# Kernel tuning notes

Measured on AMD Instinct MI355X. Metric: run time of the kernel, lower is better.

The kernel has to match this reference:

```python
import jax, jax.numpy as jnp
import numpy as np

B, T = 48, 88200          # batch of 2 s clips at internal_sr=44100
N_EXC, N_LOOP = 6, 2      # exc_order+1, loop_order+1


def invert_lpc(y, A):
    """x[t] = y[t] + sum_{k=1..N} A[:, t, k-1] * y[t-k]  (zi = 0).
    y: (B,T), A: (B,T,N) -> (B,T). Vectorized time-varying FIR."""
    Bs, Ts = y.shape
    N = A.shape[2]
    yp = jnp.pad(y, ((0, 0), (N, 0)))  # N leading zeros = zero initial state
    # shifts[:, t, k-1] = y[t-k]
    shifts = jnp.stack([yp[:, N - k:N - k + Ts] for k in range(1, N + 1)], axis=2)
    return y + jnp.sum(A * shifts, axis=2)


def sample_wise_lpc(x, A):
    """Time-varying all-pole IIR: y[t] = x[t] - sum_{k=1..N} A[:, t, k-1]*y[t-k].
    Sequential recurrence over T via lax.scan. x: (B,T), A: (B,T,N)."""
    Bs, Ts = x.shape
    N = A.shape[2]

    def step(carry, inp):
        # carry: (B,N) = [y[t-1], ..., y[t-N]]
        xt, at = inp  # (B,), (B,N)
        yt = xt - jnp.sum(at * carry, axis=1)
        new_carry = jnp.concatenate([yt[:, None], carry[:, :-1]], axis=1)
        return new_carry, yt

    carry0 = jnp.zeros((Bs, N), x.dtype)
    _, ys = jax.lax.scan(step, carry0, (x.T, jnp.swapaxes(A, 0, 1)))
    return ys.T  # (B,T)


def setup_inputs() -> dict:
    key = jax.random.key(0)
    k1, k2, k3 = jax.random.split(key, 3)
    y = jax.random.normal(k1, (B, T), dtype=jnp.float32)
    # excitation (FIR-inverse) coefficients: mild, zero-centered
    A_exc = (jax.random.uniform(k2, (B, T, N_EXC), dtype=jnp.float32) - 0.5) * 0.2
    # loop (all-pole) coefficients kept small so the IIR recurrence is stable
    A_loop = (jax.random.uniform(k3, (B, T, N_LOOP), dtype=jnp.float32) - 0.5) * 0.5
    return {"y": y, "A_exc": A_exc, "A_loop": A_loop}


def reference(y, A_exc, A_loop):
    # Core DiffKS pipeline kernel: inverse LPC (feed-forward comb/loop inversion)
    # followed by the sample-wise recursive LPC resynthesis (Karplus-Strong loop).
    x = invert_lpc(y, A_exc)
    return sample_wise_lpc(x, A_loop)
```

## Files before the change

kernel.cpp:

```cpp
#include <hip/hip_runtime.h>


#define T_LEN 88200
#define B_N   48
#define OUT_W 224
#define WUP   32
#define NCH   394
#define WPB   4

__device__ __forceinline__ float4 zero4() { return make_float4(0.f, 0.f, 0.f, 0.f); }

__device__ __forceinline__ float4 ld_guard(const float* p, int t) {
    if (t >= 0 && t + 3 < T_LEN) return *(const float4*)(p + t);
    return zero4();
}

__global__ __launch_bounds__(256, 5) void diffks_kernel(
    const float* __restrict__ y, const float* __restrict__ A_exc,
    const float* __restrict__ A_loop, float* __restrict__ out) {
    const int tid  = threadIdx.x;
    const int widx = tid >> 6;
    const int lane = tid & 63;
    const int w = blockIdx.x * WPB + widx;
    const int b = w / NCH;
    const int c = w - b * NCH;
    const int s  = c * OUT_W;
    const int w0 = s - WUP;
    const int t0 = w0 + 4 * lane;

    const float* yb  = y      + (size_t)b * T_LEN;
    const float* aeb = A_exc  + (size_t)b * T_LEN * 6;
    const float* alb = A_loop + (size_t)b * T_LEN * 2;
    float*       ob  = out    + (size_t)b * T_LEN;

    const bool valid = (t0 >= 0) && (t0 + 3 < T_LEN);
    float4 yv, ae0, ae1, ae2, ae3, ae4, ae5, al0, al1;
    if (valid) {
        yv = *(const float4*)(yb + t0);
        const float4* pae = (const float4*)(aeb + (size_t)t0 * 6);
        ae0 = pae[0]; ae1 = pae[1]; ae2 = pae[2];
        ae3 = pae[3]; ae4 = pae[4]; ae5 = pae[5];
        const float4* pal = (const float4*)(alb + (size_t)t0 * 2);
        al0 = pal[0]; al1 = pal[1];
    } else {
        yv = ae0 = ae1 = ae2 = ae3 = ae4 = ae5 = al0 = al1 = zero4();
    }

    float4 ymid, ylo;
    ymid.x = __shfl_up(yv.x, 1, 64); ymid.y = __shfl_up(yv.y, 1, 64);
    ymid.z = __shfl_up(yv.z, 1, 64); ymid.w = __shfl_up(yv.w, 1, 64);
    ylo.x  = __shfl_up(yv.x, 2, 64); ylo.y  = __shfl_up(yv.y, 2, 64);
    ylo.z  = __shfl_up(yv.z, 2, 64); ylo.w  = __shfl_up(yv.w, 2, 64);
    if (lane == 0) ymid = ld_guard(yb, t0 - 4);
    if (lane <= 1) ylo  = ld_guard(yb, t0 - 8);

    float yw[12] = { ylo.x, ylo.y, ylo.z, ylo.w,
                     ymid.x, ymid.y, ymid.z, ymid.w,
                     yv.x, yv.y, yv.z, yv.w };
    float aef[24] = { ae0.x, ae0.y, ae0.z, ae0.w, ae1.x, ae1.y, ae1.z, ae1.w,
                      ae2.x, ae2.y, ae2.z, ae2.w, ae3.x, ae3.y, ae3.z, ae3.w,
                      ae4.x, ae4.y, ae4.z, ae4.w, ae5.x, ae5.y, ae5.z, ae5.w };
    float alf[8]  = { al0.x, al0.y, al0.z, al0.w, al1.x, al1.y, al1.z, al1.w };

    float xs[4], a1s[4], a2s[4];
    float p00 = 1.f, p01 = 0.f, p10 = 0.f, p11 = 1.f, c0 = 0.f, c1 = 0.f;
#pragma unroll
    for (int j = 0; j < 4; ++j) {
        float xv = yw[8 + j];
#pragma unroll
        for (int k = 1; k <= 6; ++k)
            xv = fmaf(aef[j * 6 + (k - 1)], yw[8 + j - k], xv);
        xs[j] = xv;
        const float a1 = alf[j * 2], a2 = alf[j * 2 + 1];
        a1s[j] = a1; a2s[j] = a2;
        const float n00 = fmaf(-a1, p00, -a2 * p10);
        const float n01 = fmaf(-a1, p01, -a2 * p11);
        p10 = p00; p11 = p01; p00 = n00; p01 = n01;
        const float nc0 = fmaf(-a1, c0, fmaf(-a2, c1, xv));
        c1 = c0; c0 = nc0;
    }

#pragma unroll
    for (int d = 1; d <= 4; d <<= 1) {
        const float q00 = __shfl_up(p00, d, 64), q01 = __shfl_up(p01, d, 64);
        const float q10 = __shfl_up(p10, d, 64), q11 = __shfl_up(p11, d, 64);
        const float qc0 = __shfl_up(c0, d, 64),  qc1 = __shfl_up(c1, d, 64);
        if (lane >= d) {
            const float m00 = fmaf(p00, q00, p01 * q10);
            const float m01 = fmaf(p00, q01, p01 * q11);
            const float m10 = fmaf(p10, q00, p11 * q10);
            const float m11 = fmaf(p10, q01, p11 * q11);
            const float nc0 = fmaf(p00, qc0, fmaf(p01, qc1, c0));
            const float nc1 = fmaf(p10, qc0, fmaf(p11, qc1, c1));
            p00 = m00; p01 = m01; p10 = m10; p11 = m11; c0 = nc0; c1 = nc1;
        }
    }
    {
        const float qc0 = __shfl_up(c0, 8, 64), qc1 = __shfl_up(c1, 8, 64);
        if (lane >= 8) {
            const float nc0 = fmaf(p00, qc0, fmaf(p01, qc1, c0));
            const float nc1 = fmaf(p10, qc0, fmaf(p11, qc1, c1));
            c0 = nc0; c1 = nc1;
        }
    }

    float y1 = __shfl_up(c0, 1, 64);
    float y2 = __shfl_up(c1, 1, 64);
    if (lane == 0) { y1 = 0.f; y2 = 0.f; }
    float ov[4];
#pragma unroll
    for (int j = 0; j < 4; ++j) {
        const float yt = fmaf(-a1s[j], y1, fmaf(-a2s[j], y2, xs[j]));
        y2 = y1; y1 = yt;
        ov[j] = yt;
    }

    if (lane >= 8 && t0 < T_LEN)
        *(float4*)(ob + t0) = make_float4(ov[0], ov[1], ov[2], ov[3]);
}

extern "C" void kernel_launch(void* const* d_in, const int* in_sizes, int n_in,
                              void* d_out, int out_size, void* d_ws, size_t ws_size,
                              hipStream_t stream) {
    const float* y      = (const float*)d_in[0];
    const float* A_exc  = (const float*)d_in[1];
    const float* A_loop = (const float*)d_in[2];
    float* out = (float*)d_out;

    const int waves = B_N * NCH;
    const int grid  = waves / WPB;
    diffks_kernel<<<grid, 256, 0, stream>>>(y, A_exc, A_loop, out);
}
```

Measured before the change: 190.1 us.

## Process eight samples per lane to widen chunks and cut warm-up overhead

Each lane now handles 8 consecutive samples instead of 4, so a wave covers 480 output samples per chunk rather than 224. The fixed 32-sample warm-up is amortized over more outputs, which cuts redundant loads and compute, and the scan needs fewer shuffle steps. Halo y values are now loaded directly from memory instead of shuffled from neighbouring lanes. Register pressure per lane rises, so the occupancy hint is lowered from 5 to 4 blocks per CU, and fewer waves are launched.

```diff
diff --git a/kernel.cpp b/kernel.cpp
--- a/kernel.cpp
+++ b/kernel.cpp
@@ -3,19 +3,19 @@
 
 #define T_LEN 88200
 #define B_N   48
-#define OUT_W 224
+#define OUT_W 480
 #define WUP   32
-#define NCH   394
+#define NCH   184
 #define WPB   4
 
 __device__ __forceinline__ float4 zero4() { return make_float4(0.f, 0.f, 0.f, 0.f); }
 
-__device__ __forceinline__ float4 ld_guard(const float* p, int t) {
+__device__ __forceinline__ float4 ld_g(const float* __restrict__ p, int t) {
     if (t >= 0 && t + 3 < T_LEN) return *(const float4*)(p + t);
     return zero4();
 }
 
-__global__ __launch_bounds__(256, 5) void diffks_kernel(
+__global__ __launch_bounds__(256, 4) void diffks_kernel(
     const float* __restrict__ y, const float* __restrict__ A_exc,
     const float* __restrict__ A_loop, float* __restrict__ out) {
     const int tid  = threadIdx.x;
@@ -25,53 +25,49 @@
     const int b = w / NCH;
     const int c = w - b * NCH;
     const int s  = c * OUT_W;
-    const int w0 = s - WUP;
-    const int t0 = w0 + 4 * lane;
+    const int t0 = s - WUP + 8 * lane;
 
     const float* yb  = y      + (size_t)b * T_LEN;
     const float* aeb = A_exc  + (size_t)b * T_LEN * 6;
     const float* alb = A_loop + (size_t)b * T_LEN * 2;
     float*       ob  = out    + (size_t)b * T_LEN;
 
-    const bool valid = (t0 >= 0) && (t0 + 3 < T_LEN);
-    float4 yv, ae0, ae1, ae2, ae3, ae4, ae5, al0, al1;
-    if (valid) {
-        yv = *(const float4*)(yb + t0);
-        const float4* pae = (const float4*)(aeb + (size_t)t0 * 6);
-        ae0 = pae[0]; ae1 = pae[1]; ae2 = pae[2];
-        ae3 = pae[3]; ae4 = pae[4]; ae5 = pae[5];
-        const float4* pal = (const float4*)(alb + (size_t)t0 * 2);
-        al0 = pal[0]; al1 = pal[1];
+    const bool full = (t0 >= 0) && (t0 < T_LEN);
+    float4 ya, yc, ae[12], al[4];
+    if (full) {
+        const float4* py = (const float4*)(yb + t0);
+        ya = py[0]; yc = py[1];
+        const float4* pa = (const float4*)(aeb + (size_t)t0 * 6);
+#pragma unroll
+        for (int i = 0; i < 12; ++i) ae[i] = pa[i];
+        const float4* pl = (const float4*)(alb + (size_t)t0 * 2);
+#pragma unroll
+        for (int i = 0; i < 4; ++i) al[i] = pl[i];
     } else {
-        yv = ae0 = ae1 = ae2 = ae3 = ae4 = ae5 = al0 = al1 = zero4();
+        ya = yc = zero4();
+#pragma unroll
+        for (int i = 0; i < 12; ++i) ae[i] = zero4();
+#pragma unroll
+        for (int i = 0; i < 4; ++i) al[i] = zero4();
     }
+    const float4 hm2 = ld_g(yb, t0 - 8);
+    const float4 hm1 = ld_g(yb, t0 - 4);
 
-    float4 ymid, ylo;
-    ymid.x = __shfl_up(yv.x, 1, 64); ymid.y = __shfl_up(yv.y, 1, 64);
-    ymid.z = __shfl_up(yv.z, 1, 64); ymid.w = __shfl_up(yv.w, 1, 64);
-    ylo.x  = __shfl_up(yv.x, 2, 64); ylo.y  = __shfl_up(yv.y, 2, 64);
-    ylo.z  = __shfl_up(yv.z, 2, 64); ylo.w  = __shfl_up(yv.w, 2, 64);
-    if (lane == 0) ymid = ld_guard(yb, t0 - 4);
-    if (lane <= 1) ylo  = ld_guard(yb, t0 - 8);
+    float yw[16] = { hm2.x, hm2.y, hm2.z, hm2.w, hm1.x, hm1.y, hm1.z, hm1.w,
+                     ya.x,  ya.y,  ya.z,  ya.w,  yc.x,  yc.y,  yc.z,  yc.w };
+    const float* aef = (const float*)ae;
+    const float* alf = (const float*)al;
 
-    float yw[12] = { ylo.x, ylo.y, ylo.z, ylo.w,
-                     ymid.x, ymid.y, ymid.z, ymid.w,
-                     yv.x, yv.y, yv.z, yv.w };
-    float aef[24] = { ae0.x, ae0.y, ae0.z, ae0.w, ae1.x, ae1.y, ae1.z, ae1.w,
-                      ae2.x, ae2.y, ae2.z, ae2.w, ae3.x, ae3.y, ae3.z, ae3.w,
-                      ae4.x, ae4.y, ae4.z, ae4.w, ae5.x, ae5.y, ae5.z, ae5.w };
-    float alf[8]  = { al0.x, al0.y, al0.z, al0.w, al1.x, al1.y, al1.z, al1.w };
-
-    float xs[4], a1s[4], a2s[4];
+    float xs[8], a1s[8], a2s[8];
     float p00 = 1.f, p01 = 0.f, p10 = 0.f, p11 = 1.f, c0 = 0.f, c1 = 0.f;
 #pragma unroll
-    for (int j = 0; j < 4; ++j) {
+    for (int j = 0; j < 8; ++j) {
         float xv = yw[8 + j];
 #pragma unroll
         for (int k = 1; k <= 6; ++k)
             xv = fmaf(aef[j * 6 + (k - 1)], yw[8 + j - k], xv);
         xs[j] = xv;
-        const float a1 = alf[j * 2], a2 = alf[j * 2 + 1];
+        const float a1 = alf[2 * j], a2 = alf[2 * j + 1];
         a1s[j] = a1; a2s[j] = a2;
         const float n00 = fmaf(-a1, p00, -a2 * p10);
         const float n01 = fmaf(-a1, p01, -a2 * p11);
@@ -81,7 +77,7 @@
     }
 
 #pragma unroll
-    for (int d = 1; d <= 4; d <<= 1) {
+    for (int d = 1; d <= 2; d <<= 1) {
         const float q00 = __shfl_up(p00, d, 64), q01 = __shfl_up(p01, d, 64);
         const float q10 = __shfl_up(p10, d, 64), q11 = __shfl_up(p11, d, 64);
         const float qc0 = __shfl_up(c0, d, 64),  qc1 = __shfl_up(c1, d, 64);
@@ -96,8 +92,8 @@
         }
     }
     {
-        const float qc0 = __shfl_up(c0, 8, 64), qc1 = __shfl_up(c1, 8, 64);
-        if (lane >= 8) {
+        const float qc0 = __shfl_up(c0, 4, 64), qc1 = __shfl_up(c1, 4, 64);
+        if (lane >= 4) {
             const float nc0 = fmaf(p00, qc0, fmaf(p01, qc1, c0));
             const float nc1 = fmaf(p10, qc0, fmaf(p11, qc1, c1));
             c0 = nc0; c1 = nc1;
@@ -107,16 +103,18 @@
     float y1 = __shfl_up(c0, 1, 64);
     float y2 = __shfl_up(c1, 1, 64);
     if (lane == 0) { y1 = 0.f; y2 = 0.f; }
-    float ov[4];
+    float ov[8];
 #pragma unroll
-    for (int j = 0; j < 4; ++j) {
+    for (int j = 0; j < 8; ++j) {
         const float yt = fmaf(-a1s[j], y1, fmaf(-a2s[j], y2, xs[j]));
         y2 = y1; y1 = yt;
         ov[j] = yt;
     }
 
-    if (lane >= 8 && t0 < T_LEN)
-        *(float4*)(ob + t0) = make_float4(ov[0], ov[1], ov[2], ov[3]);
+    if (lane >= WUP / 8 && t0 < T_LEN) {
+        *(float4*)(ob + t0)     = make_float4(ov[0], ov[1], ov[2], ov[3]);
+        *(float4*)(ob + t0 + 4) = make_float4(ov[4], ov[5], ov[6], ov[7]);
+    }
 }
 
 extern "C" void kernel_launch(void* const* d_in, const int* in_sizes, int n_in,
```

New measurement: 194.5 us. 2.3% more time.

## Split fused FIR+IIR into separate FIR and IIR kernels via workspace

Applied to the files above, without the earlier changes.

Splits the single fused kernel into a FIR kernel that writes the excitation signal x to the workspace and an IIR kernel that reads x back and runs the scan. The FIR pass no longer recomputes the warm-up overlap, so each A_exc element is read once instead of being re-read across overlapping chunk windows. In exchange, x costs an extra global write and read, plus a second kernel launch. The fused kernel is kept as a fallback when the workspace is too small. The final store guard also changes from t0 < T_LEN to t0 + 3 < T_LEN.

```diff
diff --git a/kernel.cpp b/kernel.cpp
--- a/kernel.cpp
+++ b/kernel.cpp
@@ -3,6 +3,8 @@
 
 #define T_LEN 88200
 #define B_N   48
+
+#define WPR   345
 #define OUT_W 224
 #define WUP   32
 #define NCH   394
@@ -10,12 +12,145 @@
 
 __device__ __forceinline__ float4 zero4() { return make_float4(0.f, 0.f, 0.f, 0.f); }
 
-__device__ __forceinline__ float4 ld_guard(const float* p, int t) {
+__device__ __forceinline__ float4 ld_g(const float* __restrict__ p, int t) {
     if (t >= 0 && t + 3 < T_LEN) return *(const float4*)(p + t);
     return zero4();
 }
 
-__global__ __launch_bounds__(256, 5) void diffks_kernel(
+__global__ __launch_bounds__(256) void fir_kernel(
+    const float* __restrict__ y, const float* __restrict__ A_exc,
+    float* __restrict__ x) {
+    const int tid  = threadIdx.x;
+    const int widx = tid >> 6;
+    const int lane = tid & 63;
+    const int w = blockIdx.x * 4 + widx;
+    const int b = w / WPR;
+    const int r = w - b * WPR;
+    const int t0 = (r * 64 + lane) * 4;
+
+    const float* yb  = y     + (size_t)b * T_LEN;
+    const float* aeb = A_exc + (size_t)b * T_LEN * 6;
+    float*       xb  = x     + (size_t)b * T_LEN;
+
+    const bool valid = (t0 + 3 < T_LEN);
+    float4 yv, ae[6];
+    if (valid) {
+        yv = *(const float4*)(yb + t0);
+        const float4* pa = (const float4*)(aeb + (size_t)t0 * 6);
+#pragma unroll
+        for (int i = 0; i < 6; ++i) ae[i] = pa[i];
+    } else {
+        yv = zero4();
+#pragma unroll
+        for (int i = 0; i < 6; ++i) ae[i] = zero4();
+    }
+
+    float4 hm1, hm2;
+    hm1.x = __shfl_up(yv.x, 1, 64); hm1.y = __shfl_up(yv.y, 1, 64);
+    hm1.z = __shfl_up(yv.z, 1, 64); hm1.w = __shfl_up(yv.w, 1, 64);
+    hm2.x = __shfl_up(yv.x, 2, 64); hm2.y = __shfl_up(yv.y, 2, 64);
+    hm2.z = __shfl_up(yv.z, 2, 64); hm2.w = __shfl_up(yv.w, 2, 64);
+    if (lane == 0) hm1 = ld_g(yb, t0 - 4);
+    if (lane <= 1) hm2 = ld_g(yb, t0 - 8);
+
+    const float yw[12] = { hm2.x, hm2.y, hm2.z, hm2.w,
+                           hm1.x, hm1.y, hm1.z, hm1.w,
+                           yv.x,  yv.y,  yv.z,  yv.w };
+    const float* aef = (const float*)ae;
+
+    float xv[4];
+#pragma unroll
+    for (int j = 0; j < 4; ++j) {
+        float acc = yw[8 + j];
+#pragma unroll
+        for (int k = 1; k <= 6; ++k)
+            acc = fmaf(aef[j * 6 + (k - 1)], yw[8 + j - k], acc);
+        xv[j] = acc;
+    }
+    if (valid)
+        *(float4*)(xb + t0) = make_float4(xv[0], xv[1], xv[2], xv[3]);
+}
+
+__global__ __launch_bounds__(256) void iir_kernel(
+    const float* __restrict__ x, const float* __restrict__ A_loop,
+    float* __restrict__ out) {
+    const int tid  = threadIdx.x;
+    const int widx = tid >> 6;
+    const int lane = tid & 63;
+    const int w = blockIdx.x * WPB + widx;
+    const int b = w / NCH;
+    const int c = w - b * NCH;
+    const int s  = c * OUT_W;
+    const int t0 = s - WUP + 4 * lane;
+
+    const float* xb  = x      + (size_t)b * T_LEN;
+    const float* alb = A_loop + (size_t)b * T_LEN * 2;
+    float*       ob  = out    + (size_t)b * T_LEN;
+
+    float4 xv4, al0, al1;
+    if (t0 >= 0 && t0 + 3 < T_LEN) {
+        xv4 = *(const float4*)(xb + t0);
+        const float4* pl = (const float4*)(alb + (size_t)t0 * 2);
+        al0 = pl[0]; al1 = pl[1];
+    } else {
+        xv4 = al0 = al1 = zero4();
+    }
+    const float xs[4]  = { xv4.x, xv4.y, xv4.z, xv4.w };
+    const float alf[8] = { al0.x, al0.y, al0.z, al0.w,
+                           al1.x, al1.y, al1.z, al1.w };
+
+    float a1s[4], a2s[4];
+    float p00 = 1.f, p01 = 0.f, p10 = 0.f, p11 = 1.f, c0 = 0.f, c1 = 0.f;
+#pragma unroll
+    for (int j = 0; j < 4; ++j) {
+        const float a1 = alf[2 * j], a2 = alf[2 * j + 1];
+        a1s[j] = a1; a2s[j] = a2;
+        const float n00 = fmaf(-a1, p00, -a2 * p10);
+        const float n01 = fmaf(-a1, p01, -a2 * p11);
+        p10 = p00; p11 = p01; p00 = n00; p01 = n01;
+        const float nc0 = fmaf(-a1, c0, fmaf(-a2, c1, xs[j]));
+        c1 = c0; c0 = nc0;
+    }
+
+#pragma unroll
+    for (int d = 1; d <= 4; d <<= 1) {
+        const float q00 = __shfl_up(p00, d, 64), q01 = __shfl_up(p01, d, 64);
+        const float q10 = __shfl_up(p10, d, 64), q11 = __shfl_up(p11, d, 64);
+        const float qc0 = __shfl_up(c0, d, 64),  qc1 = __shfl_up(c1, d, 64);
+        if (lane >= d) {
+            const float m00 = fmaf(p00, q00, p01 * q10);
+            const float m01 = fmaf(p00, q01, p01 * q11);
+            const float m10 = fmaf(p10, q00, p11 * q10);
+            const float m11 = fmaf(p10, q01, p11 * q11);
+            const float nc0 = fmaf(p00, qc0, fmaf(p01, qc1, c0));
+            const float nc1 = fmaf(p10, qc0, fmaf(p11, qc1, c1));
+            p00 = m00; p01 = m01; p10 = m10; p11 = m11; c0 = nc0; c1 = nc1;
+        }
+    }
+    {
+        const float qc0 = __shfl_up(c0, 8, 64), qc1 = __shfl_up(c1, 8, 64);
+        if (lane >= 8) {
+            const float nc0 = fmaf(p00, qc0, fmaf(p01, qc1, c0));
+            const float nc1 = fmaf(p10, qc0, fmaf(p11, qc1, c1));
+            c0 = nc0; c1 = nc1;
+        }
+    }
+
+    float y1 = __shfl_up(c0, 1, 64);
+    float y2 = __shfl_up(c1, 1, 64);
+    if (lane == 0) { y1 = 0.f; y2 = 0.f; }
+    float ov[4];
+#pragma unroll
+    for (int j = 0; j < 4; ++j) {
+        const float yt = fmaf(-a1s[j], y1, fmaf(-a2s[j], y2, xs[j]));
+        y2 = y1; y1 = yt;
+        ov[j] = yt;
+    }
+    if (lane >= WUP / 4 && t0 + 3 < T_LEN)
+        *(float4*)(ob + t0) = make_float4(ov[0], ov[1], ov[2], ov[3]);
+}
+
+__global__ __launch_bounds__(256) void fused_kernel(
     const float* __restrict__ y, const float* __restrict__ A_exc,
     const float* __restrict__ A_loop, float* __restrict__ out) {
     const int tid  = threadIdx.x;
@@ -25,8 +160,7 @@
     const int b = w / NCH;
     const int c = w - b * NCH;
     const int s  = c * OUT_W;
-    const int w0 = s - WUP;
-    const int t0 = w0 + 4 * lane;
+    const int t0 = s - WUP + 4 * lane;
 
     const float* yb  = y      + (size_t)b * T_LEN;
     const float* aeb = A_exc  + (size_t)b * T_LEN * 6;
@@ -34,34 +168,32 @@
     float*       ob  = out    + (size_t)b * T_LEN;
 
     const bool valid = (t0 >= 0) && (t0 + 3 < T_LEN);
-    float4 yv, ae0, ae1, ae2, ae3, ae4, ae5, al0, al1;
+    float4 yv, ae[6], al0, al1;
     if (valid) {
         yv = *(const float4*)(yb + t0);
-        const float4* pae = (const float4*)(aeb + (size_t)t0 * 6);
-        ae0 = pae[0]; ae1 = pae[1]; ae2 = pae[2];
-        ae3 = pae[3]; ae4 = pae[4]; ae5 = pae[5];
-        const float4* pal = (const float4*)(alb + (size_t)t0 * 2);
-        al0 = pal[0]; al1 = pal[1];
-    } else {
-        yv = ae0 = ae1 = ae2 = ae3 = ae4 = ae5 = al0 = al1 = zero4();
-    }
-
-    float4 ymid, ylo;
-    ymid.x = __shfl_up(yv.x, 1, 64); ymid.y = __shfl_up(yv.y, 1, 64);
-    ymid.z = __shfl_up(yv.z, 1, 64); ymid.w = __shfl_up(yv.w, 1, 64);
-    ylo.x  = __shfl_up(yv.x, 2, 64); ylo.y  = __shfl_up(yv.y, 2, 64);
-    ylo.z  = __shfl_up(yv.z, 2, 64); ylo.w  = __shfl_up(yv.w, 2, 64);
-    if (lane == 0) ymid = ld_guard(yb, t0 - 4);
-    if (lane <= 1) ylo  = ld_guard(yb, t0 - 8);
-
-    float yw[12] = { ylo.x, ylo.y, ylo.z, ylo.w,
-                     ymid.x, ymid.y, ymid.z, ymid.w,
-                     yv.x, yv.y, yv.z, yv.w };
-    float aef[24] = { ae0.x, ae0.y, ae0.z, ae0.w, ae1.x, ae1.y, ae1.z, ae1.w,
-                      ae2.x, ae2.y, ae2.z, ae2.w, ae3.x, ae3.y, ae3.z, ae3.w,
-                      ae4.x, ae4.y, ae4.z, ae4.w, ae5.x, ae5.y, ae5.z, ae5.w };
-    float alf[8]  = { al0.x, al0.y, al0.z, al0.w, al1.x, al1.y, al1.z, al1.w };
-
+        const float4* pa = (const float4*)(aeb + (size_t)t0 * 6);
+#pragma unroll
+        for (int i = 0; i < 6; ++i) ae[i] = pa[i];
+        const float4* pl = (const float4*)(alb + (size_t)t0 * 2);
+        al0 = pl[0]; al1 = pl[1];
+    } else {
+        yv = al0 = al1 = zero4();
+#pragma unroll
+        for (int i = 0; i < 6; ++i) ae[i] = zero4();
+    }
+    float4 hm1, hm2;
+    hm1.x = __shfl_up(yv.x, 1, 64); hm1.y = __shfl_up(yv.y, 1, 64);
+    hm1.z = __shfl_up(yv.z, 1, 64); hm1.w = __shfl_up(yv.w, 1, 64);
+    hm2.x = __shfl_up(yv.x, 2, 64); hm2.y = __shfl_up(yv.y, 2, 64);
+    hm2.z = __shfl_up(yv.z, 2, 64); hm2.w = __shfl_up(yv.w, 2, 64);
+    if (lane == 0) hm1 = ld_g(yb, t0 - 4);
+    if (lane <= 1) hm2 = ld_g(yb, t0 - 8);
+    const float yw[12] = { hm2.x, hm2.y, hm2.z, hm2.w,
+                           hm1.x, hm1.y, hm1.z, hm1.w,
+                           yv.x, yv.y, yv.z, yv.w };
+    const float* aef = (const float*)ae;
+    const float alf[8] = { al0.x, al0.y, al0.z, al0.w,
+                           al1.x, al1.y, al1.z, al1.w };
     float xs[4], a1s[4], a2s[4];
     float p00 = 1.f, p01 = 0.f, p10 = 0.f, p11 = 1.f, c0 = 0.f, c1 = 0.f;
 #pragma unroll
@@ -71,7 +203,7 @@
         for (int k = 1; k <= 6; ++k)
             xv = fmaf(aef[j * 6 + (k - 1)], yw[8 + j - k], xv);
         xs[j] = xv;
-        const float a1 = alf[j * 2], a2 = alf[j * 2 + 1];
+        const float a1 = alf[2 * j], a2 = alf[2 * j + 1];
         a1s[j] = a1; a2s[j] = a2;
         const float n00 = fmaf(-a1, p00, -a2 * p10);
         const float n01 = fmaf(-a1, p01, -a2 * p11);
@@ -79,7 +211,6 @@
         const float nc0 = fmaf(-a1, c0, fmaf(-a2, c1, xv));
         c1 = c0; c0 = nc0;
     }
-
 #pragma unroll
     for (int d = 1; d <= 4; d <<= 1) {
         const float q00 = __shfl_up(p00, d, 64), q01 = __shfl_up(p01, d, 64);
@@ -103,7 +234,6 @@
             c0 = nc0; c1 = nc1;
         }
     }
-
     float y1 = __shfl_up(c0, 1, 64);
     float y2 = __shfl_up(c1, 1, 64);
     if (lane == 0) { y1 = 0.f; y2 = 0.f; }
@@ -114,8 +244,7 @@
         y2 = y1; y1 = yt;
         ov[j] = yt;
     }
-
-    if (lane >= 8 && t0 < T_LEN)
+    if (lane >= WUP / 4 && t0 + 3 < T_LEN)
         *(float4*)(ob + t0) = make_float4(ov[0], ov[1], ov[2], ov[3]);
 }
 
@@ -127,7 +256,15 @@
     const float* A_loop = (const float*)d_in[2];
     float* out = (float*)d_out;
 
-    const int waves = B_N * NCH;
-    const int grid  = waves / WPB;
-    diffks_kernel<<<grid, 256, 0, stream>>>(y, A_exc, A_loop, out);
-}
+    const size_t x_bytes = (size_t)B_N * T_LEN * sizeof(float);
+    if (ws_size >= x_bytes) {
+        float* x = (float*)d_ws;
+        const int wavesA = B_N * WPR;
+        fir_kernel<<<wavesA / 4, 256, 0, stream>>>(y, A_exc, x);
+        const int wavesB = B_N * NCH;
+        iir_kernel<<<wavesB / WPB, 256, 0, stream>>>(x, A_loop, out);
+    } else {
+        const int waves = B_N * NCH;
+        fused_kernel<<<waves / WPB, 256, 0, stream>>>(y, A_exc, A_loop, out);
+    }
+}
```

Result: no change. 191.3 us (+0.6%).
